# Performance work log

Measured on AMD Instinct MI355X. Metric: run time of the kernel, lower is better.

The kernel has to match this reference:

```python
import jax, jax.numpy as jnp
import numpy as np


def setup_inputs() -> dict:
    key = jax.random.key(0)
    k1, k2, k3 = jax.random.split(key, 3)
    n_nodes, n_attrs, n_edges, n_known = 100000, 50, 1600000, 50000
    x = jax.random.normal(k1, (n_nodes, n_attrs), dtype=jnp.float32)
    edge_index = jax.random.randint(k2, (2, n_edges), 0, n_nodes, dtype=jnp.int32)
    know_mask = jax.random.randint(k3, (n_known,), 0, n_nodes, dtype=jnp.int32)
    eta = jnp.zeros((n_attrs,), dtype=jnp.float32)
    theta = jnp.zeros((n_attrs,), dtype=jnp.float32)
    return {"x": x, "eta": eta, "theta": theta, "edge_index": edge_index,
            "know_mask": know_mask, "num_iter": 30}


def reference(x, eta, theta, edge_index, know_mask, num_iter):
    n = x.shape[0]
    row, col = edge_index[0], edge_index[1]
    # sym-normalized adjacency weights: D^{-1/2} A D^{-1/2} (get_laplacian 'sym'
    # followed by remove_self_loops(-w) leaves exactly the normalized adjacency)
    deg = jax.ops.segment_sum(jnp.ones(row.shape[0], x.dtype), row, num_segments=n)
    dinv = jnp.where(deg > 0, jax.lax.rsqrt(jnp.where(deg > 0, deg, 1.0)), 0.0)
    w = dinv[row] * dinv[col]  # [E]

    # is_binary=False -> mean over known rows, std = 1
    mean = x[know_mask].mean(axis=0)          # [d]
    out_k_init = x[know_mask] - mean          # [K, d]
    # initial out is detached in the original (clone().detach())
    out0 = jax.lax.stop_gradient(jnp.zeros_like(x).at[know_mask].set(x[know_mask]))
    out0 = out0 - mean

    nf = float(n)
    alpha = (nf - 1.0) / (theta * nf + (nf - 1.0))   # [d]
    inv_a = 1.0 / alpha
    beta = inv_a / (inv_a + eta)                      # [d]

    def step(out, _):
        # spmm(adj, out): gather by col, scale, scatter-add by row
        agg = jax.ops.segment_sum(w[:, None] * out[col], row, num_segments=n)
        out = alpha * agg + (1.0 - alpha) * out.mean(axis=0)
        out = out.at[know_mask].set(beta * out[know_mask] + (1.0 - beta) * out_k_init)
        return out, None

    out, _ = jax.lax.scan(step, out0, None, length=num_iter)
    return out + mean  # * std (=1)
```

## Files before the change

kernel.cpp:

```cpp
#include <hip/hip_runtime.h>
#include <hip/hip_fp16.h>


#define NUM_ITER 30

union U8 { uint2 u; __half2 h[2]; };

__global__ __launch_bounds__(256) void k_deg(const int* __restrict__ row,
                                             int* __restrict__ deg, int E) {
    int e = blockIdx.x * 256 + threadIdx.x;
    if (e < E) atomicAdd(&deg[__builtin_nontemporal_load(row + e)], 1);
}

__global__ __launch_bounds__(1024) void k_scanA(const int* __restrict__ deg,
                                                int* __restrict__ blocksum, int n) {
    __shared__ int sdata[1024];
    int i = blockIdx.x * 1024 + threadIdx.x;
    int v = (i < n) ? deg[i] : 0;
    sdata[threadIdx.x] = v;
    __syncthreads();
    for (int s = 512; s > 0; s >>= 1) {
        if (threadIdx.x < s) sdata[threadIdx.x] += sdata[threadIdx.x + s];
        __syncthreads();
    }
    if (threadIdx.x == 0) blocksum[blockIdx.x] = sdata[0];
}

__global__ __launch_bounds__(1024) void k_scanC(const int* __restrict__ deg,
                                                const int* __restrict__ blocksum,
                                                int* __restrict__ rowptr,
                                                int* __restrict__ cursor,
                                                float* __restrict__ dinv, int n, int E) {
    __shared__ int soff;
    __shared__ int sdata[1024];
    int tid = threadIdx.x;
    if (tid == 0) {
        int o = 0;
        for (int b = 0; b < (int)blockIdx.x; b++) o += blocksum[b];
        soff = o;
    }
    int i = blockIdx.x * 1024 + tid;
    int v = (i < n) ? deg[i] : 0;
    sdata[tid] = v;
    __syncthreads();
    for (int s = 1; s < 1024; s <<= 1) {
        int t = (tid >= s) ? sdata[tid - s] : 0;
        __syncthreads();
        sdata[tid] += t;
        __syncthreads();
    }
    if (i < n) {
        int rp = soff + sdata[tid] - v;
        rowptr[i] = rp;
        cursor[i] = rp;
        dinv[i] = (v > 0) ? (1.0f / sqrtf((float)v)) : 0.0f;
    }
    if (i == 0) rowptr[n] = E;
}

__global__ __launch_bounds__(256) void k_fill(const int* __restrict__ row,
                                              const int* __restrict__ col,
                                              int* __restrict__ cursor,
                                              int* __restrict__ csrc, int E, int n) {
    const int grp = blockIdx.x & 7;
    const int nb = gridDim.x >> 3;
    const int bi = blockIdx.x >> 3;
    const int lo = (int)(((long long)grp * n) >> 3);
    const int hi = (int)(((long long)(grp + 1) * n) >> 3);
    for (int e = bi * 256 + threadIdx.x; e < E; e += nb * 256) {
        int r = __builtin_nontemporal_load(row + e);
        if (r >= lo && r < hi) {
            int c = __builtin_nontemporal_load(col + e);
            int pos = atomicAdd(&cursor[r], 1);
            csrc[pos] = c;
        }
    }
}

__global__ __launch_bounds__(256) void k_flags(const int* __restrict__ km,
                                               int* __restrict__ is_known, int K) {
    int k = blockIdx.x * 256 + threadIdx.x;
    if (k < K) is_known[km[k]] = 1;
}

__global__ __launch_bounds__(256) void k_mean(const float* __restrict__ x,
                                              const int* __restrict__ km,
                                              float* __restrict__ msum, int K, int d) {
    int lane = threadIdx.x & 63, wv = threadIdx.x >> 6;
    int wglob = blockIdx.x * 4 + wv;
    int stride = gridDim.x * 4;
    float s = 0.f;
    for (int k = wglob; k < K; k += stride) {
        int idx = km[k];
        if (lane < d) s += x[(size_t)idx * d + lane];
    }
    __shared__ float red[4][64];
    red[wv][lane] = s;
    __syncthreads();
    if (wv == 0) {
        float t = red[0][lane] + red[1][lane] + red[2][lane] + red[3][lane];
        if (lane < d) atomicAdd(&msum[lane], t);
    }
}

__global__ __launch_bounds__(64) void k_ab(const float* __restrict__ eta,
                                           const float* __restrict__ theta,
                                           const float* __restrict__ msum,
                                           float* __restrict__ ab, float* __restrict__ meanv,
                                           int n, int d, int K) {
    int j = threadIdx.x;
    float a = 1.f, b = 1.f, m = 0.f;
    if (j < d) {
        float nf = (float)n;
        float th = theta[j], et = eta[j];
        a = (nf - 1.f) / (th * nf + (nf - 1.f));
        float ia = 1.f / a;
        b = ia / (ia + et);
        m = msum[j] / (float)K;
    }
    ab[j] = a;
    ab[64 + j] = b;
    meanv[j] = m;
    int nc = __any(a != 1.0f);
    int nk = __any(b != 1.0f);
    if (j == 0) {
        int* abf = (int*)(ab + 128);
        abf[0] = nc;
        abf[1] = nk;
    }
}

__global__ __launch_bounds__(256) void k_init(uint2* __restrict__ outA,
                                              uint2* __restrict__ outB,
                                              const int* __restrict__ is_known,
                                              const float* __restrict__ x,
                                              const float* __restrict__ meanv,
                                              const float* __restrict__ dinv,
                                              float* __restrict__ partials0, int n, int d) {
    int lane = threadIdx.x & 63, wv = threadIdx.x >> 6;
    int r = blockIdx.x * 4 + wv;
    float val = 0.f, scaled = 0.f;
    if (r < n) {
        float mn = meanv[lane];
        float xv = (is_known[r] && lane < d) ? x[(size_t)r * d + lane] : 0.f;
        val = xv - mn;
        scaled = val * dinv[r];
    }
    float a0 = __shfl(scaled, (lane & 15) * 4);
    float a1 = __shfl(scaled, (lane & 15) * 4 + 1);
    float a2 = __shfl(scaled, (lane & 15) * 4 + 2);
    float a3 = __shfl(scaled, (lane & 15) * 4 + 3);
    if (r <= n && lane < 16) {
        U8 o;
        o.h[0] = __floats2half2_rn(a0, a1);
        o.h[1] = __floats2half2_rn(a2, a3);
        outA[(size_t)r * 16 + lane] = o.u;
        if (r == n) outB[(size_t)r * 16 + lane] = o.u;
    }
    __shared__ float red[4][64];
    red[wv][lane] = (r < n) ? val : 0.f;
    __syncthreads();
    if (wv == 0) {
        float s = red[0][lane] + red[1][lane] + red[2][lane] + red[3][lane];
        atomicAdd(&partials0[(blockIdx.x & 255) * 64 + lane], s);
    }
}

__global__ __launch_bounds__(1024) void k_fin(const float* __restrict__ partials,
                                              float* __restrict__ colsum_out,
                                              const int* __restrict__ flag) {
    if (flag[0] == 0) return;
    int tid = threadIdx.x;
    int c = tid & 15;
    int s = tid >> 4;
    const float4* p4 = (const float4*)partials;
    float4 acc = {0.f, 0.f, 0.f, 0.f};
    for (int k = 0; k < 4; k++) {
        float4 v = p4[(s * 4 + k) * 16 + c];
        acc.x += v.x; acc.y += v.y; acc.z += v.z; acc.w += v.w;
    }
    __shared__ float4 red[64][16];
    red[s][c] = acc;
    __syncthreads();
    for (int st = 32; st >= 1; st >>= 1) {
        if (s < st) {
            float4 o = red[s + st][c];
            red[s][c].x += o.x; red[s][c].y += o.y;
            red[s][c].z += o.z; red[s][c].w += o.w;
        }
        __syncthreads();
    }
    if (tid < 16) ((float4*)colsum_out)[c] = red[0][c];
}

__global__ __launch_bounds__(256) void k_spmm(const uint2* __restrict__ in,
                                              void* __restrict__ out,
                                              const int* __restrict__ csrc,
                                              const int* __restrict__ rowptr,
                                              const float* __restrict__ dinv,
                                              const float* __restrict__ ab,
                                              const float* __restrict__ colsum_t,
                                              float* __restrict__ partials_next,
                                              const int* __restrict__ is_known,
                                              const float* __restrict__ x,
                                              const float* __restrict__ meanv,
                                              int n, int d, int final_packed) {
    const int tid = threadIdx.x;
    const int lane = tid & 63;
    const int wv = tid >> 6;
    const int g = lane >> 4;
    const int c = lane & 15;
    const int r = blockIdx.x * 4 + wv;

    const int* abf = (const int*)(ab + 128);
    const int need_cs = abf[0];
    const int need_kb = abf[1];

    float4 acc = {0.f, 0.f, 0.f, 0.f};
    const int rr = __builtin_amdgcn_readfirstlane(r);

    if (r < n) {
        const int e0 = rowptr[rr];
        const int e1 = rowptr[rr + 1];
        const int deg = e1 - e0;
        int col_l = n;
        if (lane < deg) col_l = csrc[e0 + lane];
        const int kmax = (deg < 64) ? deg : 64;
        for (int base = 0; base < kmax; base += 16) {
            int s0 = base + g;
            int c0 = __shfl(col_l, s0);
            int c1 = __shfl(col_l, s0 + 4);
            int c2 = __shfl(col_l, s0 + 8);
            int c3 = __shfl(col_l, s0 + 12);
            U8 v0, v1, v2, v3;
            v0.u = in[(size_t)c0 * 16 + c];
            v1.u = in[(size_t)c1 * 16 + c];
            v2.u = in[(size_t)c2 * 16 + c];
            v3.u = in[(size_t)c3 * 16 + c];
            float2 f00 = __half22float2(v0.h[0]), f01 = __half22float2(v0.h[1]);
            float2 f10 = __half22float2(v1.h[0]), f11 = __half22float2(v1.h[1]);
            float2 f20 = __half22float2(v2.h[0]), f21 = __half22float2(v2.h[1]);
            float2 f30 = __half22float2(v3.h[0]), f31 = __half22float2(v3.h[1]);
            acc.x += f00.x + f10.x + f20.x + f30.x;
            acc.y += f00.y + f10.y + f20.y + f30.y;
            acc.z += f01.x + f11.x + f21.x + f31.x;
            acc.w += f01.y + f11.y + f21.y + f31.y;
        }
        for (int e = e0 + 64 + g; e < e1; e += 4) {
            U8 v; v.u = in[(size_t)csrc[e] * 16 + c];
            float2 fa = __half22float2(v.h[0]), fb = __half22float2(v.h[1]);
            acc.x += fa.x; acc.y += fa.y; acc.z += fb.x; acc.w += fb.y;
        }
    }

    acc.x += __shfl_xor(acc.x, 16); acc.y += __shfl_xor(acc.y, 16);
    acc.z += __shfl_xor(acc.z, 16); acc.w += __shfl_xor(acc.w, 16);
    acc.x += __shfl_xor(acc.x, 32); acc.y += __shfl_xor(acc.y, 32);
    acc.z += __shfl_xor(acc.z, 32); acc.w += __shfl_xor(acc.w, 32);

    const float dr = (r < n) ? dinv[rr] : 0.f;
    float4 al4 = ((const float4*)ab)[c];
    float4 mn4 = ((const float4*)meanv)[c];
    const float inv_n = 1.0f / (float)n;

    float4 cs4 = {0.f, 0.f, 0.f, 0.f};
    if (need_cs) cs4 = ((const float4*)colsum_t)[c];

    float4 val;
    val.x = al4.x * (dr * acc.x) + (1.f - al4.x) * cs4.x * inv_n;
    val.y = al4.y * (dr * acc.y) + (1.f - al4.y) * cs4.y * inv_n;
    val.z = al4.z * (dr * acc.z) + (1.f - al4.z) * cs4.z * inv_n;
    val.w = al4.w * (dr * acc.w) + (1.f - al4.w) * cs4.w * inv_n;

    __shared__ float red[4][64];
    const int do_part = need_cs && !final_packed;
    if (do_part) red[wv][lane] = 0.f;

    if (r < n && g == 0) {
        if (need_kb && is_known[rr]) {
            float4 be4 = ((const float4*)(ab + 64))[c];
            int base = r * d, a = 4 * c;
            float x0 = (a + 0 < d) ? x[base + a + 0] : 0.f;
            float x1 = (a + 1 < d) ? x[base + a + 1] : 0.f;
            float x2 = (a + 2 < d) ? x[base + a + 2] : 0.f;
            float x3 = (a + 3 < d) ? x[base + a + 3] : 0.f;
            val.x = be4.x * val.x + (1.f - be4.x) * (x0 - mn4.x);
            val.y = be4.y * val.y + (1.f - be4.y) * (x1 - mn4.y);
            val.z = be4.z * val.z + (1.f - be4.z) * (x2 - mn4.z);
            val.w = be4.w * val.w + (1.f - be4.w) * (x3 - mn4.w);
        }
        if (!final_packed) {
            U8 o;
            o.h[0] = __floats2half2_rn(val.x * dr, val.y * dr);
            o.h[1] = __floats2half2_rn(val.z * dr, val.w * dr);
            ((uint2*)out)[(size_t)r * 16 + c] = o.u;
        } else {
            float* of = (float*)out;
            int base = r * d, a = 4 * c;
            if (a + 0 < d) of[base + a + 0] = val.x + mn4.x;
            if (a + 1 < d) of[base + a + 1] = val.y + mn4.y;
            if (a + 2 < d) of[base + a + 2] = val.z + mn4.z;
            if (a + 3 < d) of[base + a + 3] = val.w + mn4.w;
        }
        if (do_part) {
            red[wv][4 * c + 0] = val.x;
            red[wv][4 * c + 1] = val.y;
            red[wv][4 * c + 2] = val.z;
            red[wv][4 * c + 3] = val.w;
        }
    }
    if (do_part) {
        __syncthreads();
        if (wv == 0) {
            float s = red[0][lane] + red[1][lane] + red[2][lane] + red[3][lane];
            atomicAdd(&partials_next[(blockIdx.x & 255) * 64 + lane], s);
        }
    }
}

extern "C" void kernel_launch(void* const* d_in, const int* in_sizes, int n_in,
                              void* d_out, int out_size, void* d_ws, size_t ws_size,
                              hipStream_t stream) {
    const float* x = (const float*)d_in[0];
    const float* eta = (const float*)d_in[1];
    const float* theta = (const float*)d_in[2];
    const int* ei = (const int*)d_in[3];
    const int* km = (const int*)d_in[4];

    const int d = in_sizes[1];
    const int n = in_sizes[0] / d;
    const int E = in_sizes[3] / 2;
    const int K = in_sizes[4];
    const int* row = ei;
    const int* col = ei + E;

    char* p = (char*)d_ws;
    auto alloc = [&](size_t bytes) -> char* {
        char* r = p;
        p += (bytes + 255) & ~(size_t)255;
        return r;
    };
    uint2* outA = (uint2*)alloc((size_t)(n + 1) * 128);
    uint2* outB = (uint2*)alloc((size_t)(n + 1) * 128);
    int* csrc = (int*)alloc((size_t)E * 4);
    int* rowptr = (int*)alloc(((size_t)n + 1) * 4);
    int* cursor = (int*)alloc((size_t)n * 4);
    float* dinv = (float*)alloc((size_t)n * 4);
    int* blocksum = (int*)alloc(1024);
    float* ab = (float*)alloc(768);
    float* meanv = (float*)alloc(256);
    float* colsum = (float*)alloc((size_t)(NUM_ITER + 1) * 64 * 4);
    char* zstart = p;
    int* deg = (int*)alloc((size_t)n * 4);
    int* is_known = (int*)alloc((size_t)n * 4);
    float* msum = (float*)alloc(256);
    float* partials = (float*)alloc((size_t)(NUM_ITER + 1) * 256 * 64 * 4);
    size_t zbytes = (size_t)(p - zstart);
    hipMemsetAsync(zstart, 0, zbytes, stream);

    const int* abf = (const int*)(ab + 128);

    const int eb = (E + 255) / 256;
    const int sb = (n + 1023) / 1024;
    const int rb = (n + 3) / 4;
    const int rb2 = (n + 1 + 3) / 4;

    k_deg<<<eb, 256, 0, stream>>>(row, deg, E);
    k_scanA<<<sb, 1024, 0, stream>>>(deg, blocksum, n);
    k_scanC<<<sb, 1024, 0, stream>>>(deg, blocksum, rowptr, cursor, dinv, n, E);
    k_fill<<<4096, 256, 0, stream>>>(row, col, cursor, csrc, E, n);
    k_flags<<<(K + 255) / 256, 256, 0, stream>>>(km, is_known, K);
    k_mean<<<512, 256, 0, stream>>>(x, km, msum, K, d);
    k_ab<<<1, 64, 0, stream>>>(eta, theta, msum, ab, meanv, n, d, K);
    k_init<<<rb2, 256, 0, stream>>>(outA, outB, is_known, x, meanv, dinv,
                                    partials, n, d);
    k_fin<<<1, 1024, 0, stream>>>(partials, colsum, abf);

    uint2* bufs[2] = {outA, outB};
    for (int t = 0; t < NUM_ITER; t++) {
        const uint2* in = bufs[t & 1];
        const int last = (t == NUM_ITER - 1);
        void* out = last ? d_out : (void*)bufs[(t + 1) & 1];
        k_spmm<<<rb, 256, 0, stream>>>(in, out, csrc, rowptr, dinv, ab,
                                       colsum + (size_t)t * 64,
                                       partials + (size_t)(t + 1) * 256 * 64,
                                       is_known, x, meanv, n, d, last);
        if (!last)
            k_fin<<<1, 1024, 0, stream>>>(partials + (size_t)(t + 1) * 256 * 64,
                                          colsum + (size_t)(t + 1) * 64, abf);
    }
}
```

Baseline: 1.424 ms.

## Fuse column-sum finalize into SpMM via block-0 reduction and spin flag

Removes the separate per-iteration k_fin reduction kernel. Block 0 of each k_spmm launch now reduces the previous iteration's partial column sums and publishes them with a release flag, while the other blocks spin on that flag before using the column mean. k_init's partial accumulation is also skipped when the column-sum term is not needed. This cuts 30 small launches, but adds an inter-block spin-wait that depends on block 0 being scheduled and makes it serialize the reduction before its own row work.

```diff
diff --git a/kernel.cpp b/kernel.cpp
--- a/kernel.cpp
+++ b/kernel.cpp
@@ -136,6 +136,7 @@
                                               const float* __restrict__ x,
                                               const float* __restrict__ meanv,
                                               const float* __restrict__ dinv,
+                                              const float* __restrict__ ab,
                                               float* __restrict__ partials0, int n, int d) {
     int lane = threadIdx.x & 63, wv = threadIdx.x >> 6;
     int r = blockIdx.x * 4 + wv;
@@ -157,40 +158,16 @@
         outA[(size_t)r * 16 + lane] = o.u;
         if (r == n) outB[(size_t)r * 16 + lane] = o.u;
     }
-    __shared__ float red[4][64];
-    red[wv][lane] = (r < n) ? val : 0.f;
-    __syncthreads();
-    if (wv == 0) {
-        float s = red[0][lane] + red[1][lane] + red[2][lane] + red[3][lane];
-        atomicAdd(&partials0[(blockIdx.x & 255) * 64 + lane], s);
-    }
-}
-
-__global__ __launch_bounds__(1024) void k_fin(const float* __restrict__ partials,
-                                              float* __restrict__ colsum_out,
-                                              const int* __restrict__ flag) {
-    if (flag[0] == 0) return;
-    int tid = threadIdx.x;
-    int c = tid & 15;
-    int s = tid >> 4;
-    const float4* p4 = (const float4*)partials;
-    float4 acc = {0.f, 0.f, 0.f, 0.f};
-    for (int k = 0; k < 4; k++) {
-        float4 v = p4[(s * 4 + k) * 16 + c];
-        acc.x += v.x; acc.y += v.y; acc.z += v.z; acc.w += v.w;
-    }
-    __shared__ float4 red[64][16];
-    red[s][c] = acc;
-    __syncthreads();
-    for (int st = 32; st >= 1; st >>= 1) {
-        if (s < st) {
-            float4 o = red[s + st][c];
-            red[s][c].x += o.x; red[s][c].y += o.y;
-            red[s][c].z += o.z; red[s][c].w += o.w;
-        }
-        __syncthreads();
-    }
-    if (tid < 16) ((float4*)colsum_out)[c] = red[0][c];
+    const int* abf = (const int*)(ab + 128);
+    if (abf[0]) {
+        __shared__ float red[4][64];
+        red[wv][lane] = (r < n) ? val : 0.f;
+        __syncthreads();
+        if (wv == 0) {
+            float s = red[0][lane] + red[1][lane] + red[2][lane] + red[3][lane];
+            atomicAdd(&partials0[(blockIdx.x & 255) * 64 + lane], s);
+        }
+    }
 }
 
 __global__ __launch_bounds__(256) void k_spmm(const uint2* __restrict__ in,
@@ -199,7 +176,9 @@
                                               const int* __restrict__ rowptr,
                                               const float* __restrict__ dinv,
                                               const float* __restrict__ ab,
-                                              const float* __restrict__ colsum_t,
+                                              const float* __restrict__ partials_cur,
+                                              float* __restrict__ colsum_t,
+                                              int* __restrict__ flag_t,
                                               float* __restrict__ partials_next,
                                               const int* __restrict__ is_known,
                                               const float* __restrict__ x,
@@ -215,6 +194,21 @@
     const int* abf = (const int*)(ab + 128);
     const int need_cs = abf[0];
     const int need_kb = abf[1];
+
+    __shared__ float red[4][64];
+
+    if (need_cs && blockIdx.x == 0) {
+        float s = 0.f;
+        for (int slot = wv; slot < 256; slot += 4)
+            s += partials_cur[slot * 64 + lane];
+        red[wv][lane] = s;
+        __syncthreads();
+        if (wv == 0)
+            colsum_t[lane] = red[0][lane] + red[1][lane] + red[2][lane] + red[3][lane];
+        __syncthreads();
+        if (tid == 0)
+            __hip_atomic_store(flag_t, 1, __ATOMIC_RELEASE, __HIP_MEMORY_SCOPE_AGENT);
+    }
 
     float4 acc = {0.f, 0.f, 0.f, 0.f};
     const int rr = __builtin_amdgcn_readfirstlane(r);
@@ -264,7 +258,17 @@
     const float inv_n = 1.0f / (float)n;
 
     float4 cs4 = {0.f, 0.f, 0.f, 0.f};
-    if (need_cs) cs4 = ((const float4*)colsum_t)[c];
+    if (need_cs) {
+        if (blockIdx.x != 0) {
+            if (tid == 0) {
+                while (__hip_atomic_load(flag_t, __ATOMIC_RELAXED,
+                                         __HIP_MEMORY_SCOPE_AGENT) == 0) {}
+            }
+            __syncthreads();
+            __builtin_amdgcn_fence(__ATOMIC_ACQUIRE, "agent");
+        }
+        cs4 = ((const float4*)colsum_t)[c];
+    }
 
     float4 val;
     val.x = al4.x * (dr * acc.x) + (1.f - al4.x) * cs4.x * inv_n;
@@ -272,7 +276,6 @@
     val.z = al4.z * (dr * acc.z) + (1.f - al4.z) * cs4.z * inv_n;
     val.w = al4.w * (dr * acc.w) + (1.f - al4.w) * cs4.w * inv_n;
 
-    __shared__ float red[4][64];
     const int do_part = need_cs && !final_packed;
     if (do_part) red[wv][lane] = 0.f;
 
@@ -300,13 +303,17 @@
             if (a + 0 < d) of[base + a + 0] = val.x + mn4.x;
             if (a + 1 < d) of[base + a + 1] = val.y + mn4.y;
             if (a + 2 < d) of[base + a + 2] = val.z + mn4.z;
-            if (a + 3 < d) of[base + a + 3] = val.w + mn4.w;
         }
         if (do_part) {
             red[wv][4 * c + 0] = val.x;
             red[wv][4 * c + 1] = val.y;
             red[wv][4 * c + 2] = val.z;
             red[wv][4 * c + 3] = val.w;
+        }
+        if (final_packed) {
+            float* of = (float*)out;
+            int base = r * d, a = 4 * c;
+            if (a + 3 < d) of[base + a + 3] = val.w + mn4.w;
         }
     }
     if (do_part) {
@@ -354,11 +361,10 @@
     int* deg = (int*)alloc((size_t)n * 4);
     int* is_known = (int*)alloc((size_t)n * 4);
     float* msum = (float*)alloc(256);
+    int* iterflags = (int*)alloc((size_t)(NUM_ITER + 1) * 4);
     float* partials = (float*)alloc((size_t)(NUM_ITER + 1) * 256 * 64 * 4);
     size_t zbytes = (size_t)(p - zstart);
     hipMemsetAsync(zstart, 0, zbytes, stream);
-
-    const int* abf = (const int*)(ab + 128);
 
     const int eb = (E + 255) / 256;
     const int sb = (n + 1023) / 1024;
@@ -372,9 +378,8 @@
     k_flags<<<(K + 255) / 256, 256, 0, stream>>>(km, is_known, K);
     k_mean<<<512, 256, 0, stream>>>(x, km, msum, K, d);
     k_ab<<<1, 64, 0, stream>>>(eta, theta, msum, ab, meanv, n, d, K);
-    k_init<<<rb2, 256, 0, stream>>>(outA, outB, is_known, x, meanv, dinv,
+    k_init<<<rb2, 256, 0, stream>>>(outA, outB, is_known, x, meanv, dinv, ab,
                                     partials, n, d);
-    k_fin<<<1, 1024, 0, stream>>>(partials, colsum, abf);
 
     uint2* bufs[2] = {outA, outB};
     for (int t = 0; t < NUM_ITER; t++) {
@@ -382,11 +387,10 @@
         const int last = (t == NUM_ITER - 1);
         void* out = last ? d_out : (void*)bufs[(t + 1) & 1];
         k_spmm<<<rb, 256, 0, stream>>>(in, out, csrc, rowptr, dinv, ab,
+                                       partials + (size_t)t * 256 * 64,
                                        colsum + (size_t)t * 64,
+                                       iterflags + t,
                                        partials + (size_t)(t + 1) * 256 * 64,
                                        is_known, x, meanv, n, d, last);
-        if (!last)
-            k_fin<<<1, 1024, 0, stream>>>(partials + (size_t)(t + 1) * 256 * 64,
-                                          colsum + (size_t)(t + 1) * 64, abf);
-    }
-}
+    }
+}
```

New measurement: 1.406 ms. About the same (-1.3%).
